# Optimization experiments

Measured on AMD Instinct MI355X. Metric: run time of the kernel, lower is better.

The kernel has to match this reference:

```python
import jax, jax.numpy as jnp
import numpy as np

B, N, D = 16, 512, 256
PH, UH, UPH = 8, 4, 4          # P_GAT heads, U_GAT heads, UP_GAT heads
P_LAYERS, U_LAYERS = 2, 1
FH, NC = 128, 2                # final hidden, num classes
N_TRAIT = 4


def setup_inputs() -> dict:
    key = jax.random.key(0)
    keys = iter(jax.random.split(key, 64))

    def rn(shape, s=0.05):
        return jax.random.normal(next(keys), shape, dtype=jnp.float32) * s

    inp = {
        "p_mask": jnp.ones((B, N), jnp.float32),
        "feature": rn((B, N, D), 1.0),
        "c_node": rn((B, 1, D), 1.0),
        "pgat_W": rn((D, D)),
        "pgat_attn": rn((PH, 2 * (D // PH))),
    }
    for i in range(1, 5):
        inp[f"up{i}_qw"] = rn((D, D))
        inp[f"up{i}_qb"] = rn((D,))
        inp[f"up{i}_kw"] = rn((D, D))
        inp[f"up{i}_kb"] = rn((D,))
        inp[f"up{i}_ow"] = rn((D, D * UPH))
        inp[f"up{i}_ob"] = rn((D,))
    inp["ugat_W"] = rn((D, D))
    inp["ugat_attn"] = rn((UH, 2 * (D // UH)))
    inp["mlp_w1"] = rn((FH, D))
    inp["mlp_b1"] = rn((FH,))
    inp["mlp_w2"] = rn((FH, FH))
    inp["mlp_b2"] = rn((FH,))
    for i in range(1, 5):
        inp[f"fcf{i}_w"] = rn((NC, FH))
        inp[f"fcf{i}_b"] = rn((NC,))
    return inp


def _mh_gat(feature, W, attn_w, n_head, num_layers, adj=None):
    """Shared math of P_GAT / U_GAT.
    attn(cat([q_i, k_j]))[..., h, h] decomposes into q_i.wq_h + k_j.wk_h,
    identical math to the broadcast-concat-linear-diagonal in the source."""
    Bx, Nx, d = feature.shape
    dh = d // n_head
    wq, wk = attn_w[:, :dh], attn_w[:, dh:]           # [h, dh] each
    for _ in range(num_layers):
        qk = (feature @ W.T).reshape(Bx, Nx, n_head, dh)
        sq = jnp.einsum('bqhd,hd->bqh', qk, wq)
        sk = jnp.einsum('bkhd,hd->bkh', qk, wk)
        scores = jnp.tanh(sq[:, :, None, :] + sk[:, None, :, :])  # [B,q,k,h]
        if adj is not None:
            scores = jnp.where(adj[:, :, :, None] == 0, jnp.float32(-1e-8), scores)
        att = jax.nn.softmax(scores, axis=-2)          # softmax over k
        hid = jnp.tanh(jnp.einsum('bqkh,bkhd->bqhd', att, qk))
        feature = feature + hid.reshape(Bx, Nx, d)
    return feature


def _up_gat(p_mask, p_feat, u_feat, qw, qb, kw, kb, ow, ob):
    """UP_GAT: all heads/layers share params & inputs -> identical heads."""
    d = p_feat.shape[-1]
    q = u_feat @ qw.T + qb                             # [B,1,D]
    k = p_feat @ kw.T + kb                             # [B,Np,D]
    sim = jnp.einsum('bqd,bkd->bqk', q, k) / jnp.sqrt(jnp.float32(d))
    sim = jnp.where(p_mask[:, None, :] == 0, jnp.float32(1e-8), sim)
    att = jax.nn.softmax(sim, axis=2)
    head = att @ p_feat                                # [B,1,D]
    mh = jnp.concatenate([head] * UPH, axis=-1)        # concat of identical heads
    return (mh @ ow.T + ob)[:, 0, :]                   # squeeze(1)


def reference(p_mask, feature, c_node, pgat_W, pgat_attn,
              up1_qw, up1_qb, up1_kw, up1_kb, up1_ow, up1_ob,
              up2_qw, up2_qb, up2_kw, up2_kb, up2_ow, up2_ob,
              up3_qw, up3_qb, up3_kw, up3_kb, up3_ow, up3_ob,
              up4_qw, up4_qb, up4_kw, up4_kb, up4_ow, up4_ob,
              ugat_W, ugat_attn, mlp_w1, mlp_b1, mlp_w2, mlp_b2,
              fcf1_w, fcf1_b, fcf2_w, fcf2_b, fcf3_w, fcf3_b, fcf4_w, fcf4_b):
    Bx = p_mask.shape[0]
    adj = p_mask[:, :, None] * p_mask[:, None, :]      # [B,N,N]
    new_p = _mh_gat(feature, pgat_W, pgat_attn, PH, P_LAYERS, adj=adj)
    new_mask = jnp.concatenate([p_mask, jnp.ones((Bx, 1), p_mask.dtype)], axis=1)
    comb = jnp.concatenate([new_p, c_node], axis=1)    # [B,N+1,D]

    u1 = _up_gat(new_mask, comb, c_node, up1_qw, up1_qb, up1_kw, up1_kb, up1_ow, up1_ob)
    u2 = _up_gat(new_mask, comb, c_node, up2_qw, up2_qb, up2_kw, up2_kb, up2_ow, up2_ob)
    u3 = _up_gat(new_mask, comb, c_node, up3_qw, up3_qb, up3_kw, up3_kb, up3_ow, up3_ob)
    u4 = _up_gat(new_mask, comb, c_node, up4_qw, up4_qb, up4_kw, up4_kb, up4_ow, up4_ob)

    u = jnp.stack([u1, u2, u3, u4], axis=1)            # [B,4,D]
    u = _mh_gat(u, ugat_W, ugat_attn, UH, U_LAYERS, adj=None)

    def mlp(x):  # fcs1..4 share modules in the torch source
        h = jax.nn.relu(x @ mlp_w1.T + mlp_b1)
        return jax.nn.relu(h @ mlp_w2.T + mlp_b2)

    heads = [(fcf1_w, fcf1_b), (fcf2_w, fcf2_b), (fcf3_w, fcf3_b), (fcf4_w, fcf4_b)]
    logits = [mlp(u[:, i]) @ w.T + b for i, (w, b) in enumerate(heads)]
    return jnp.stack(logits, axis=0)                   # [4,B,NC]
```

## Files before the change

### kernel.cpp

```cpp
#include <hip/hip_runtime.h>

constexpr int CB   = 16;
constexpr int CN   = 512;
constexpr int CD   = 256;
constexpr int CPH  = 8;
constexpr int CDH  = 32;
constexpr int CNP1 = 513;
constexpr int CFH  = 128;
constexpr int CNC  = 2;

typedef __bf16 bf16x8 __attribute__((ext_vector_type(8)));
typedef float  f32x4  __attribute__((ext_vector_type(4)));

__device__ __forceinline__ float tanh_fast(float x) {
  x = fminf(fmaxf(x, -15.f), 15.f);
  float e = __expf(2.f * x);
  return (e - 1.f) / (e + 1.f);
}

__global__ __launch_bounds__(256) void gemm_bf16s(
    const float* __restrict__ A, const float* __restrict__ W,
    float* __restrict__ C)
{
  const int t  = threadIdx.x;
  const int nt = blockIdx.x * 64;
  const int mt = blockIdx.y * 64;
  const int wv = t >> 6, ln = t & 63;
  const int quad = ln >> 4, lc = ln & 15;

  __shared__ __align__(16) __bf16 aHi[64][56];
  __shared__ __align__(16) __bf16 aLo[64][56];
  __shared__ __align__(16) __bf16 bHi[64][56];
  __shared__ __align__(16) __bf16 bLo[64][56];

  f32x4 acc[4];
#pragma unroll
  for (int j = 0; j < 4; j++)
#pragma unroll
    for (int r = 0; r < 4; r++) acc[j][r] = 0.f;

  const int sr  = t >> 2;
  const int skq = (t & 3) * 8;

  for (int k0 = 0; k0 < 256; k0 += 32) {
    __syncthreads();
    {
      const float* ap = A + (size_t)(mt + sr) * 256 + k0 + skq;
      const float* wp = W + (size_t)(nt + sr) * 256 + k0 + skq;
      float4 a0 = *(const float4*)ap, a1 = *(const float4*)(ap + 4);
      float4 w0 = *(const float4*)wp, w1 = *(const float4*)(wp + 4);
      float av[8] = {a0.x, a0.y, a0.z, a0.w, a1.x, a1.y, a1.z, a1.w};
      float wvv[8] = {w0.x, w0.y, w0.z, w0.w, w1.x, w1.y, w1.z, w1.w};
      bf16x8 ah, al, bh, bl;
#pragma unroll
      for (int j = 0; j < 8; j++) {
        ah[j] = (__bf16)av[j];
        al[j] = (__bf16)(av[j] - (float)ah[j]);
        bh[j] = (__bf16)wvv[j];
        bl[j] = (__bf16)(wvv[j] - (float)bh[j]);
      }
      *(bf16x8*)&aHi[sr][skq] = ah;
      *(bf16x8*)&aLo[sr][skq] = al;
      *(bf16x8*)&bHi[sr][skq] = bh;
      *(bf16x8*)&bLo[sr][skq] = bl;
    }
    __syncthreads();
    bf16x8 fah = *(const bf16x8*)&aHi[wv * 16 + lc][quad * 8];
    bf16x8 fal = *(const bf16x8*)&aLo[wv * 16 + lc][quad * 8];
#pragma unroll
    for (int j = 0; j < 4; j++) {
      bf16x8 fbh = *(const bf16x8*)&bHi[j * 16 + lc][quad * 8];
      bf16x8 fbl = *(const bf16x8*)&bLo[j * 16 + lc][quad * 8];
      acc[j] = __builtin_amdgcn_mfma_f32_16x16x32_bf16(fah, fbh, acc[j], 0, 0, 0);
      acc[j] = __builtin_amdgcn_mfma_f32_16x16x32_bf16(fah, fbl, acc[j], 0, 0, 0);
      acc[j] = __builtin_amdgcn_mfma_f32_16x16x32_bf16(fal, fbh, acc[j], 0, 0, 0);
    }
  }
#pragma unroll
  for (int j = 0; j < 4; j++)
#pragma unroll
    for (int r = 0; r < 4; r++)
      C[(size_t)(mt + wv * 16 + quad * 4 + r) * 256 + nt + j * 16 + lc] = acc[j][r];
}

__global__ __launch_bounds__(256) void pgat_sqsk(
    const float* __restrict__ qk, const float* __restrict__ attnw,
    float* __restrict__ sqT, float* __restrict__ skT)
{
  __shared__ float aw[CPH * 64];
  const int t = threadIdx.x;
  for (int i = t; i < CPH * 64; i += 256) aw[i] = attnw[i];
  __syncthreads();
  const int r = blockIdx.x * 32 + (t >> 3);
  const int h = t & 7;
  const float* p  = qk + (size_t)r * CD + h * CDH;
  const float* w1 = &aw[h * 64];
  const float* w2 = &aw[h * 64 + 32];
  float s1 = 0.f, s2 = 0.f;
#pragma unroll
  for (int j = 0; j < CDH; j += 4) {
    float4 v = *(const float4*)(p + j);
    s1 += v.x * w1[j] + v.y * w1[j + 1] + v.z * w1[j + 2] + v.w * w1[j + 3];
    s2 += v.x * w2[j] + v.y * w2[j + 1] + v.z * w2[j + 2] + v.w * w2[j + 3];
  }
  const int b = r >> 9, n = r & 511;
  sqT[((size_t)b * CPH + h) * CN + n] = s1;
  skT[((size_t)b * CPH + h) * CN + n] = s2;
}

__global__ __launch_bounds__(256) void pgat_attn_mfma(
    const float* __restrict__ qk, const float* __restrict__ sqT,
    const float* __restrict__ skT, const float* __restrict__ pmask,
    const float* __restrict__ fin, float* __restrict__ fout, int outStride)
{
  const int qt = blockIdx.x;
  const int h  = blockIdx.y;
  const int b  = blockIdx.z;
  const int t  = threadIdx.x;
  const int wv = t >> 6;
  const int ln = t & 63;
  const int quad = ln >> 4;
  const int lc   = ln & 15;

  __shared__ __align__(16) __bf16 pbuf[64][72];
  __shared__ __align__(16) __bf16 vbuf[32][72];
  __shared__ float skl[CN];
  __shared__ float pml[CN];
  __shared__ float sql[64];
  __shared__ float pmq[64];

  for (int i = t; i < CN; i += 256) {
    skl[i] = skT[((size_t)b * CPH + h) * CN + i];
    pml[i] = pmask[b * CN + i];
  }
  if (t < 64) {
    sql[t] = sqT[((size_t)b * CPH + h) * CN + qt * 64 + t];
    pmq[t] = pmask[b * CN + qt * 64 + t];
  }

  f32x4 accV0 = {0.f, 0.f, 0.f, 0.f};
  f32x4 accV1 = {0.f, 0.f, 0.f, 0.f};
  f32x4 accD  = {0.f, 0.f, 0.f, 0.f};
  bf16x8 ones;
#pragma unroll
  for (int j = 0; j < 8; j++) ones[j] = (__bf16)1.0f;

  const int qg = t >> 2;
  const int kb = (t & 3) * 16;
  const int vkk = t >> 3;
  const int vdq = (t & 7) * 4;

  for (int k0 = 0; k0 < CN; k0 += 64) {
    __syncthreads();
    {
      float4 v0 = *(const float4*)(qk + ((size_t)(b * CN + k0 + vkk)) * CD + h * CDH + vdq);
      float4 v1 = *(const float4*)(qk + ((size_t)(b * CN + k0 + 32 + vkk)) * CD + h * CDH + vdq);
      vbuf[vdq + 0][vkk] = (__bf16)v0.x; vbuf[vdq + 1][vkk] = (__bf16)v0.y;
      vbuf[vdq + 2][vkk] = (__bf16)v0.z; vbuf[vdq + 3][vkk] = (__bf16)v0.w;
      vbuf[vdq + 0][32 + vkk] = (__bf16)v1.x; vbuf[vdq + 1][32 + vkk] = (__bf16)v1.y;
      vbuf[vdq + 2][32 + vkk] = (__bf16)v1.z; vbuf[vdq + 3][32 + vkk] = (__bf16)v1.w;
    }
    {
      float sq_ = sql[qg];
      float mq  = pmq[qg];
      bf16x8 w0, w1;
#pragma unroll
      for (int j = 0; j < 8; j++) {
        float s = tanh_fast(sq_ + skl[k0 + kb + j]);
        if (mq * pml[k0 + kb + j] == 0.f) s = -1e-8f;
        w0[j] = (__bf16)__expf(s);
      }
#pragma unroll
      for (int j = 0; j < 8; j++) {
        float s = tanh_fast(sq_ + skl[k0 + kb + 8 + j]);
        if (mq * pml[k0 + kb + 8 + j] == 0.f) s = -1e-8f;
        w1[j] = (__bf16)__expf(s);
      }
      *(bf16x8*)&pbuf[qg][kb]     = w0;
      *(bf16x8*)&pbuf[qg][kb + 8] = w1;
    }
    __syncthreads();
#pragma unroll
    for (int s = 0; s < 2; s++) {
      bf16x8 a  = *(const bf16x8*)&pbuf[wv * 16 + lc][s * 32 + quad * 8];
      bf16x8 b0 = *(const bf16x8*)&vbuf[lc][s * 32 + quad * 8];
      bf16x8 b1 = *(const bf16x8*)&vbuf[16 + lc][s * 32 + quad * 8];
      accV0 = __builtin_amdgcn_mfma_f32_16x16x32_bf16(a, b0, accV0, 0, 0, 0);
      accV1 = __builtin_amdgcn_mfma_f32_16x16x32_bf16(a, b1, accV1, 0, 0, 0);
      accD  = __builtin_amdgcn_mfma_f32_16x16x32_bf16(a, ones, accD, 0, 0, 0);
    }
  }
#pragma unroll
  for (int r = 0; r < 4; r++) {
    int q = qt * 64 + wv * 16 + quad * 4 + r;
    float inv = 1.f / accD[r];
    int d0 = h * CDH + lc;
    const float* ip = fin + ((size_t)b * CN + q) * CD;
    float*       op = fout + ((size_t)b * outStride + q) * CD;
    op[d0]      = ip[d0]      + tanh_fast(accV0[r] * inv);
    op[d0 + 16] = ip[d0 + 16] + tanh_fast(accV1[r] * inv);
  }
}


__global__ __launch_bounds__(256) void up_q_all(
    const float* __restrict__ cnode,
    const float* __restrict__ qw0, const float* __restrict__ qb0,
    const float* __restrict__ kw0, const float* __restrict__ kb0,
    const float* __restrict__ qw1, const float* __restrict__ qb1,
    const float* __restrict__ kw1, const float* __restrict__ kb1,
    const float* __restrict__ qw2, const float* __restrict__ qb2,
    const float* __restrict__ kw2, const float* __restrict__ kb2,
    const float* __restrict__ qw3, const float* __restrict__ qb3,
    const float* __restrict__ kw3, const float* __restrict__ kb3,
    float* __restrict__ qt_, float* __restrict__ qkb,
    float* __restrict__ comb, float* __restrict__ head, float* __restrict__ den)
{
  const int up = blockIdx.x, b = blockIdx.y, t = threadIdx.x;
  const float* qw = (up == 0) ? qw0 : (up == 1) ? qw1 : (up == 2) ? qw2 : qw3;
  const float* qb = (up == 0) ? qb0 : (up == 1) ? qb1 : (up == 2) ? qb2 : qb3;
  const float* kw = (up == 0) ? kw0 : (up == 1) ? kw1 : (up == 2) ? kw2 : kw3;
  const float* kb = (up == 0) ? kb0 : (up == 1) ? kb1 : (up == 2) ? kb2 : kb3;
  __shared__ float cl[CD];
  __shared__ float ql[CD];
  __shared__ float red[256];
  cl[t] = cnode[b * CD + t];
  head[((size_t)b * 4 + up) * CD + t] = 0.f;
  if (t == 0) den[b * 4 + up] = 0.f;
  __syncthreads();
  if (up == 0) comb[((size_t)b * CNP1 + CN) * CD + t] = cl[t];
  {
    const float* wr = qw + (size_t)t * CD;
    float a = qb[t];
#pragma unroll 4
    for (int k = 0; k < CD; k += 4) {
      float4 w4 = *(const float4*)(wr + k);
      a += cl[k] * w4.x + cl[k + 1] * w4.y + cl[k + 2] * w4.z + cl[k + 3] * w4.w;
    }
    ql[t] = a;
  }
  __syncthreads();
  {
    float a = 0.f;
    for (int d = 0; d < CD; d++) a += ql[d] * kw[d * CD + t];
    qt_[((size_t)up * CB + b) * CD + t] = a;
  }
  red[t] = ql[t] * kb[t];
  __syncthreads();
  for (int s = 128; s > 0; s >>= 1) { if (t < s) red[t] += red[t + s]; __syncthreads(); }
  if (t == 0) qkb[up * CB + b] = red[0];
}

__global__ __launch_bounds__(256) void up_sim(
    const float* __restrict__ comb, const float* __restrict__ qt,
    const float* __restrict__ qkb, const float* __restrict__ pmask,
    float* __restrict__ sim)
{
  const int b = blockIdx.y, t = threadIdx.x;
  const int w = t >> 6, l = t & 63;
  __shared__ float qtl[4 * CD];
  __shared__ float qkbl[4];
  for (int i = t; i < 4 * CD; i += 256)
    qtl[i] = qt[((size_t)(i >> 8) * CB + b) * CD + (i & 255)];
  if (t < 4) qkbl[t] = qkb[t * CB + b];
  __syncthreads();
  const int n = blockIdx.x * 4 + w;
  if (n >= CNP1) return;
  float4 c4 = *(const float4*)(comb + ((size_t)b * CNP1 + n) * CD + l * 4);
  float p[4];
#pragma unroll
  for (int u = 0; u < 4; u++) {
    float4 q4 = *(const float4*)&qtl[u * CD + l * 4];
    p[u] = c4.x * q4.x + c4.y * q4.y + c4.z * q4.z + c4.w * q4.w;
  }
#pragma unroll
  for (int off = 32; off > 0; off >>= 1) {
#pragma unroll
    for (int u = 0; u < 4; u++) p[u] += __shfl_xor(p[u], off);
  }
  if (l == 0) {
    float m = (n < CN) ? pmask[b * CN + n] : 1.f;
#pragma unroll
    for (int u = 0; u < 4; u++) {
      float s = (p[u] + qkbl[u]) * 0.0625f;
      if (m == 0.f) s = 1e-8f;
      sim[((size_t)b * 4 + u) * CNP1 + n] = s;
    }
  }
}

__global__ __launch_bounds__(256) void up_head(
    const float* __restrict__ comb, const float* __restrict__ sim,
    float* __restrict__ head, float* __restrict__ den)
{
  const int b = blockIdx.x, n0 = blockIdx.y * 64, t = threadIdx.x;
  const int up = t >> 6, dq = t & 63;
  __shared__ float attl[4][64];
  {
    int u = t >> 6, j = t & 63;
    attl[u][j] = (n0 + j < CNP1)
        ? __expf(sim[((size_t)b * 4 + u) * CNP1 + n0 + j]) : 0.f;
  }
  __syncthreads();
  float4 acc = make_float4(0.f, 0.f, 0.f, 0.f);
  const int nmax = min(64, CNP1 - n0);
  for (int j = 0; j < nmax; j++) {
    float a = attl[up][j];
    float4 c4 = *(const float4*)(comb + ((size_t)b * CNP1 + n0 + j) * CD + dq * 4);
    acc.x += a * c4.x; acc.y += a * c4.y; acc.z += a * c4.z; acc.w += a * c4.w;
  }
  float* hp = head + ((size_t)b * 4 + up) * CD + dq * 4;
  atomicAdd(hp + 0, acc.x); atomicAdd(hp + 1, acc.y);
  atomicAdd(hp + 2, acc.z); atomicAdd(hp + 3, acc.w);
  if (dq == 0) {
    float s = 0.f;
    for (int j = 0; j < 64; j++) s += attl[up][j];
    atomicAdd(den + b * 4 + up, s);
  }
}

__global__ __launch_bounds__(256) void up_out_all(
    const float* __restrict__ head, const float* __restrict__ den,
    const float* __restrict__ ow0, const float* __restrict__ ob0,
    const float* __restrict__ ow1, const float* __restrict__ ob1,
    const float* __restrict__ ow2, const float* __restrict__ ob2,
    const float* __restrict__ ow3, const float* __restrict__ ob3,
    float* __restrict__ uout)
{
  const int b = blockIdx.x, up = blockIdx.y, t = threadIdx.x;
  const float* ow = (up == 0) ? ow0 : (up == 1) ? ow1 : (up == 2) ? ow2 : ow3;
  const float* ob = (up == 0) ? ob0 : (up == 1) ? ob1 : (up == 2) ? ob2 : ob3;
  __shared__ float hl[CD];
  hl[t] = head[((size_t)b * 4 + up) * CD + t] * (1.f / den[b * 4 + up]);
  __syncthreads();
  const float* r0 = ow + (size_t)t * 4 * CD;
  float a = ob[t];
#pragma unroll 2
  for (int dd = 0; dd < CD; dd += 4) {
    float4 w0 = *(const float4*)(r0 + dd);
    float4 w1 = *(const float4*)(r0 + CD + dd);
    float4 w2 = *(const float4*)(r0 + 2 * CD + dd);
    float4 w3 = *(const float4*)(r0 + 3 * CD + dd);
    a += hl[dd]     * (w0.x + w1.x + w2.x + w3.x)
       + hl[dd + 1] * (w0.y + w1.y + w2.y + w3.y)
       + hl[dd + 2] * (w0.z + w1.z + w2.z + w3.z)
       + hl[dd + 3] * (w0.w + w1.w + w2.w + w3.w);
  }
  uout[((size_t)b * 4 + up) * CD + t] = a;
}

__global__ __launch_bounds__(256) void ugat_qk(
    const float* __restrict__ u, const float* __restrict__ W,
    const float* __restrict__ attnw,
    float* __restrict__ uqk, float* __restrict__ sqk)
{
  const int b = blockIdx.x, node = blockIdx.y, t = threadIdx.x;
  __shared__ float ul[CD];
  __shared__ float qkl[CD];
  ul[t] = u[((size_t)b * 4 + node) * CD + t];
  __syncthreads();
  const float* wr = W + (size_t)t * CD;
  float p0 = 0.f, p1 = 0.f, p2 = 0.f, p3 = 0.f;
#pragma unroll 4
  for (int d = 0; d < CD; d += 16) {
    float4 w0 = *(const float4*)(wr + d);
    float4 w1 = *(const float4*)(wr + d + 4);
    float4 w2 = *(const float4*)(wr + d + 8);
    float4 w3 = *(const float4*)(wr + d + 12);
    p0 += ul[d +  0] * w0.x + ul[d +  1] * w0.y + ul[d +  2] * w0.z + ul[d +  3] * w0.w;
    p1 += ul[d +  4] * w1.x + ul[d +  5] * w1.y + ul[d +  6] * w1.z + ul[d +  7] * w1.w;
    p2 += ul[d +  8] * w2.x + ul[d +  9] * w2.y + ul[d + 10] * w2.z + ul[d + 11] * w2.w;
    p3 += ul[d + 12] * w3.x + ul[d + 13] * w3.y + ul[d + 14] * w3.z + ul[d + 15] * w3.w;
  }
  float a = (p0 + p1) + (p2 + p3);
  qkl[t] = a;
  uqk[((size_t)b * 4 + node) * CD + t] = a;
  __syncthreads();
  if (t < 8) {
    const int h = t >> 1, which = t & 1;
    const float* w = attnw + h * 128 + which * 64;
    float s = 0.f;
    for (int j = 0; j < 64; j++) s += qkl[h * 64 + j] * w[j];
    sqk[(((size_t)b * 4 + node) * 4 + h) * 2 + which] = s;
  }
}

__global__ __launch_bounds__(256) void ugat_attn3(
    const float* __restrict__ uqk, const float* __restrict__ sqk,
    float* __restrict__ u)
{
  const int b = blockIdx.x, t = threadIdx.x;
  __shared__ float uq[4][CD];
  __shared__ float sl[4][4], kl[4][4];
  for (int i = t; i < 4 * CD; i += 256) uq[i >> 8][i & 255] = uqk[(size_t)b * 4 * CD + i];
  if (t < 16) {
    int node = t >> 2, h = t & 3;
    sl[node][h] = sqk[(((size_t)b * 4 + node) * 4 + h) * 2 + 0];
    kl[node][h] = sqk[(((size_t)b * 4 + node) * 4 + h) * 2 + 1];
  }
  __syncthreads();
  const int h = t >> 6;
#pragma unroll
  for (int q = 0; q < 4; q++) {
    float e[4]; float ssum = 0.f;
#pragma unroll
    for (int k = 0; k < 4; k++) { e[k] = __expf(tanh_fast(sl[q][h] + kl[k][h])); ssum += e[k]; }
    float hid = 0.f;
#pragma unroll
    for (int k = 0; k < 4; k++) hid += e[k] * uq[k][t];
    size_t idx = (size_t)b * 4 * CD + q * CD + t;
    u[idx] = u[idx] + tanh_fast(hid / ssum);
  }
}

__global__ __launch_bounds__(128) void mlp_kernel(
    const float* __restrict__ u,
    const float* __restrict__ w1, const float* __restrict__ b1,
    const float* __restrict__ w2, const float* __restrict__ b2,
    const float* __restrict__ f1w, const float* __restrict__ f1b,
    const float* __restrict__ f2w, const float* __restrict__ f2b,
    const float* __restrict__ f3w, const float* __restrict__ f3b,
    const float* __restrict__ f4w, const float* __restrict__ f4b,
    float* __restrict__ out)
{
  const int b = blockIdx.x, i = blockIdx.y, t = threadIdx.x;
  __shared__ float xl[CD];
  __shared__ float h1[CFH];
  __shared__ float h2[CFH];
  xl[t]       = u[((size_t)b * 4 + i) * CD + t];
  xl[t + 128] = u[((size_t)b * 4 + i) * CD + t + 128];
  __syncthreads();
  {
    const float* r = w1 + (size_t)t * CD;
    float a = b1[t];
#pragma unroll 4
    for (int k = 0; k < CD; k += 4) {
      float4 v = *(const float4*)(r + k);
      a += xl[k] * v.x + xl[k + 1] * v.y + xl[k + 2] * v.z + xl[k + 3] * v.w;
    }
    h1[t] = fmaxf(a, 0.f);
  }
  __syncthreads();
  {
    const float* r = w2 + (size_t)t * CFH;
    float a = b2[t];
#pragma unroll 4
    for (int k = 0; k < CFH; k += 4) {
      float4 v = *(const float4*)(r + k);
      a += h1[k] * v.x + h1[k + 1] * v.y + h1[k + 2] * v.z + h1[k + 3] * v.w;
    }
    h2[t] = fmaxf(a, 0.f);
  }
  __syncthreads();
  if (t < CNC) {
    const float* fw; const float* fb;
    switch (i) {
      case 0:  fw = f1w; fb = f1b; break;
      case 1:  fw = f2w; fb = f2b; break;
      case 2:  fw = f3w; fb = f3b; break;
      default: fw = f4w; fb = f4b; break;
    }
    const float* r = fw + (size_t)t * CFH;
    float a = fb[t];
    for (int k = 0; k < CFH; k++) a += h2[k] * r[k];
    out[(size_t)i * (CB * CNC) + b * CNC + t] = a;
  }
}

extern "C" void kernel_launch(void* const* d_in, const int* in_sizes, int n_in,
                              void* d_out, int out_size, void* d_ws, size_t ws_size,
                              hipStream_t stream) {
  (void)in_sizes; (void)n_in; (void)out_size; (void)ws_size;
  const float* pmask    = (const float*)d_in[0];
  const float* feature  = (const float*)d_in[1];
  const float* cnode    = (const float*)d_in[2];
  const float* pgat_W   = (const float*)d_in[3];
  const float* pgat_att = (const float*)d_in[4];
  const float* upw[4][6];
  for (int i = 0; i < 4; i++)
    for (int j = 0; j < 6; j++) upw[i][j] = (const float*)d_in[5 + i * 6 + j];
  const float* ugat_W   = (const float*)d_in[29];
  const float* ugat_att = (const float*)d_in[30];
  const float* mlp_w1 = (const float*)d_in[31];
  const float* mlp_b1 = (const float*)d_in[32];
  const float* mlp_w2 = (const float*)d_in[33];
  const float* mlp_b2 = (const float*)d_in[34];
  const float* fcf[8];
  for (int j = 0; j < 8; j++) fcf[j] = (const float*)d_in[35 + j];

  float* ws = (float*)d_ws;
  size_t o = 0;
  float* ws_qk   = ws + o; o += (size_t)CB * CN * CD;
  float* ws_feat = ws + o; o += (size_t)CB * CN * CD;
  float* ws_comb = ws + o; o += (size_t)CB * CNP1 * CD;
  float* ws_sq   = ws + o; o += (size_t)CB * CPH * CN;
  float* ws_sk   = ws + o; o += (size_t)CB * CPH * CN;
  float* ws_qt   = ws + o; o += (size_t)4 * CB * CD;
  float* ws_qkb  = ws + o; o += 4 * CB;
  float* ws_sim  = ws + o; o += (size_t)CB * 4 * CNP1;
  float* ws_den  = ws + o; o += CB * 4;
  float* ws_head = ws + o; o += (size_t)CB * 4 * CD;
  float* ws_u    = ws + o; o += (size_t)CB * 4 * CD;
  float* ws_uqk  = ws + o; o += (size_t)CB * 4 * CD;
  float* ws_sqk  = ws + o; o += (size_t)CB * 4 * 4 * 2;

  const dim3 gemmGrid(CD / 64, (CB * CN) / 64);
  const dim3 attnGrid(CN / 64, CPH, CB);

  gemm_bf16s<<<gemmGrid, 256, 0, stream>>>(feature, pgat_W, ws_qk);
  pgat_sqsk<<<dim3(CB * CN / 32), 256, 0, stream>>>(ws_qk, pgat_att, ws_sq, ws_sk);
  pgat_attn_mfma<<<attnGrid, 256, 0, stream>>>(ws_qk, ws_sq, ws_sk, pmask, feature, ws_feat, CN);
  gemm_bf16s<<<gemmGrid, 256, 0, stream>>>(ws_feat, pgat_W, ws_qk);
  pgat_sqsk<<<dim3(CB * CN / 32), 256, 0, stream>>>(ws_qk, pgat_att, ws_sq, ws_sk);
  pgat_attn_mfma<<<attnGrid, 256, 0, stream>>>(ws_qk, ws_sq, ws_sk, pmask, ws_feat, ws_comb, CNP1);

  up_q_all<<<dim3(4, CB), 256, 0, stream>>>(cnode,
      upw[0][0], upw[0][1], upw[0][2], upw[0][3],
      upw[1][0], upw[1][1], upw[1][2], upw[1][3],
      upw[2][0], upw[2][1], upw[2][2], upw[2][3],
      upw[3][0], upw[3][1], upw[3][2], upw[3][3],
      ws_qt, ws_qkb, ws_comb, ws_head, ws_den);
  up_sim<<<dim3((CNP1 + 3) / 4, CB), 256, 0, stream>>>(ws_comb, ws_qt, ws_qkb, pmask, ws_sim);
  up_head<<<dim3(CB, (CNP1 + 63) / 64), 256, 0, stream>>>(ws_comb, ws_sim, ws_head, ws_den);
  up_out_all<<<dim3(CB, 4), 256, 0, stream>>>(ws_head, ws_den,
      upw[0][4], upw[0][5], upw[1][4], upw[1][5],
      upw[2][4], upw[2][5], upw[3][4], upw[3][5], ws_u);

  ugat_qk<<<dim3(CB, 4), 256, 0, stream>>>(ws_u, ugat_W, ugat_att, ws_uqk, ws_sqk);
  ugat_attn3<<<dim3(CB), 256, 0, stream>>>(ws_uqk, ws_sqk, ws_u);
  mlp_kernel<<<dim3(CB, 4), 128, 0, stream>>>(ws_u, mlp_w1, mlp_b1, mlp_w2, mlp_b2,
                                              fcf[0], fcf[1], fcf[2], fcf[3],
                                              fcf[4], fcf[5], fcf[6], fcf[7],
                                              (float*)d_out);
}
```

Baseline: 323.8 us.

## Fuse score projections into GEMM epilogue, store qk as bf16, merge small kernels

The GEMM epilogue now computes the per-head sq/sk attention projections through shuffle reductions and writes qk directly as bf16, which removes the separate pgat_sqsk kernel and halves qk traffic into the attention kernel. up_sim and up_head become one kernel that computes each similarity and exponentiates it in place, dropping the sim buffer. ugat_attn3 is folded into the MLP kernel. The cost is a reduction in precision for qk, which was already rounded to bf16 inside the attention kernel, and each up_headsim thread now runs a serial 256-element dot product.

```diff
diff --git a/kernel.cpp b/kernel.cpp
--- a/kernel.cpp
+++ b/kernel.cpp
@@ -10,6 +10,7 @@
 constexpr int CNC  = 2;
 
 typedef __bf16 bf16x8 __attribute__((ext_vector_type(8)));
+typedef __bf16 bf16x4 __attribute__((ext_vector_type(4)));
 typedef float  f32x4  __attribute__((ext_vector_type(4)));
 
 __device__ __forceinline__ float tanh_fast(float x) {
@@ -18,9 +19,10 @@
   return (e - 1.f) / (e + 1.f);
 }
 
-__global__ __launch_bounds__(256) void gemm_bf16s(
+__global__ __launch_bounds__(256) void gemm_fused(
     const float* __restrict__ A, const float* __restrict__ W,
-    float* __restrict__ C)
+    const float* __restrict__ attnw, __bf16* __restrict__ C,
+    float* __restrict__ sqT, float* __restrict__ skT)
 {
   const int t  = threadIdx.x;
   const int nt = blockIdx.x * 64;
@@ -80,36 +82,47 @@
   for (int j = 0; j < 4; j++)
 #pragma unroll
     for (int r = 0; r < 4; r++)
-      C[(size_t)(mt + wv * 16 + quad * 4 + r) * 256 + nt + j * 16 + lc] = acc[j][r];
-}
-
-__global__ __launch_bounds__(256) void pgat_sqsk(
-    const float* __restrict__ qk, const float* __restrict__ attnw,
-    float* __restrict__ sqT, float* __restrict__ skT)
-{
-  __shared__ float aw[CPH * 64];
-  const int t = threadIdx.x;
-  for (int i = t; i < CPH * 64; i += 256) aw[i] = attnw[i];
-  __syncthreads();
-  const int r = blockIdx.x * 32 + (t >> 3);
-  const int h = t & 7;
-  const float* p  = qk + (size_t)r * CD + h * CDH;
-  const float* w1 = &aw[h * 64];
-  const float* w2 = &aw[h * 64 + 32];
-  float s1 = 0.f, s2 = 0.f;
-#pragma unroll
-  for (int j = 0; j < CDH; j += 4) {
-    float4 v = *(const float4*)(p + j);
-    s1 += v.x * w1[j] + v.y * w1[j + 1] + v.z * w1[j + 2] + v.w * w1[j + 3];
-    s2 += v.x * w2[j] + v.y * w2[j + 1] + v.z * w2[j + 2] + v.w * w2[j + 3];
-  }
-  const int b = r >> 9, n = r & 511;
-  sqT[((size_t)b * CPH + h) * CN + n] = s1;
-  skT[((size_t)b * CPH + h) * CN + n] = s2;
+      C[(size_t)(mt + wv * 16 + quad * 4 + r) * 256 + nt + j * 16 + lc] =
+          (__bf16)acc[j][r];
+
+  const int hA = blockIdx.x * 2, hB = hA + 1;
+  const float wqa0 = attnw[hA * 64 + lc],      wqa1 = attnw[hA * 64 + 16 + lc];
+  const float wka0 = attnw[hA * 64 + 32 + lc], wka1 = attnw[hA * 64 + 48 + lc];
+  const float wqb0 = attnw[hB * 64 + lc],      wqb1 = attnw[hB * 64 + 16 + lc];
+  const float wkb0 = attnw[hB * 64 + 32 + lc], wkb1 = attnw[hB * 64 + 48 + lc];
+  float sqa[4], ska[4], sqb[4], skb[4];
+#pragma unroll
+  for (int r = 0; r < 4; r++) {
+    sqa[r] = acc[0][r] * wqa0 + acc[1][r] * wqa1;
+    ska[r] = acc[0][r] * wka0 + acc[1][r] * wka1;
+    sqb[r] = acc[2][r] * wqb0 + acc[3][r] * wqb1;
+    skb[r] = acc[2][r] * wkb0 + acc[3][r] * wkb1;
+  }
+#pragma unroll
+  for (int m = 1; m <= 8; m <<= 1) {
+#pragma unroll
+    for (int r = 0; r < 4; r++) {
+      sqa[r] += __shfl_xor(sqa[r], m);
+      ska[r] += __shfl_xor(ska[r], m);
+      sqb[r] += __shfl_xor(sqb[r], m);
+      skb[r] += __shfl_xor(skb[r], m);
+    }
+  }
+  if (lc == 0) {
+#pragma unroll
+    for (int r = 0; r < 4; r++) {
+      int gm = mt + wv * 16 + quad * 4 + r;
+      int bb = gm >> 9, nn = gm & 511;
+      sqT[((size_t)bb * CPH + hA) * CN + nn] = sqa[r];
+      skT[((size_t)bb * CPH + hA) * CN + nn] = ska[r];
+      sqT[((size_t)bb * CPH + hB) * CN + nn] = sqb[r];
+      skT[((size_t)bb * CPH + hB) * CN + nn] = skb[r];
+    }
+  }
 }
 
 __global__ __launch_bounds__(256) void pgat_attn_mfma(
-    const float* __restrict__ qk, const float* __restrict__ sqT,
+    const __bf16* __restrict__ qk, const float* __restrict__ sqT,
     const float* __restrict__ skT, const float* __restrict__ pmask,
     const float* __restrict__ fin, float* __restrict__ fout, int outStride)
 {
@@ -153,12 +166,12 @@
   for (int k0 = 0; k0 < CN; k0 += 64) {
     __syncthreads();
     {
-      float4 v0 = *(const float4*)(qk + ((size_t)(b * CN + k0 + vkk)) * CD + h * CDH + vdq);
-      float4 v1 = *(const float4*)(qk + ((size_t)(b * CN + k0 + 32 + vkk)) * CD + h * CDH + vdq);
-      vbuf[vdq + 0][vkk] = (__bf16)v0.x; vbuf[vdq + 1][vkk] = (__bf16)v0.y;
-      vbuf[vdq + 2][vkk] = (__bf16)v0.z; vbuf[vdq + 3][vkk] = (__bf16)v0.w;
-      vbuf[vdq + 0][32 + vkk] = (__bf16)v1.x; vbuf[vdq + 1][32 + vkk] = (__bf16)v1.y;
-      vbuf[vdq + 2][32 + vkk] = (__bf16)v1.z; vbuf[vdq + 3][32 + vkk] = (__bf16)v1.w;
+      bf16x4 v0 = *(const bf16x4*)(qk + ((size_t)(b * CN + k0 + vkk)) * CD + h * CDH + vdq);
+      bf16x4 v1 = *(const bf16x4*)(qk + ((size_t)(b * CN + k0 + 32 + vkk)) * CD + h * CDH + vdq);
+      vbuf[vdq + 0][vkk] = v0[0]; vbuf[vdq + 1][vkk] = v0[1];
+      vbuf[vdq + 2][vkk] = v0[2]; vbuf[vdq + 3][vkk] = v0[3];
+      vbuf[vdq + 0][32 + vkk] = v1[0]; vbuf[vdq + 1][32 + vkk] = v1[1];
+      vbuf[vdq + 2][32 + vkk] = v1[2]; vbuf[vdq + 3][32 + vkk] = v1[3];
     }
     {
       float sq_ = sql[qg];
@@ -251,70 +264,53 @@
   if (t == 0) qkb[up * CB + b] = red[0];
 }
 
-__global__ __launch_bounds__(256) void up_sim(
+__global__ __launch_bounds__(256) void up_headsim(
     const float* __restrict__ comb, const float* __restrict__ qt,
     const float* __restrict__ qkb, const float* __restrict__ pmask,
-    float* __restrict__ sim)
-{
-  const int b = blockIdx.y, t = threadIdx.x;
-  const int w = t >> 6, l = t & 63;
-  __shared__ float qtl[4 * CD];
+    float* __restrict__ head, float* __restrict__ den)
+{
+  const int b = blockIdx.x, n0 = blockIdx.y * 64, t = threadIdx.x;
+  const int up = t >> 6, j = t & 63;
+  __shared__ float qtl[4][CD];
   __shared__ float qkbl[4];
+  __shared__ float attl[4][64];
   for (int i = t; i < 4 * CD; i += 256)
-    qtl[i] = qt[((size_t)(i >> 8) * CB + b) * CD + (i & 255)];
+    qtl[i >> 8][i & 255] = qt[((size_t)(i >> 8) * CB + b) * CD + (i & 255)];
   if (t < 4) qkbl[t] = qkb[t * CB + b];
   __syncthreads();
-  const int n = blockIdx.x * 4 + w;
-  if (n >= CNP1) return;
-  float4 c4 = *(const float4*)(comb + ((size_t)b * CNP1 + n) * CD + l * 4);
-  float p[4];
-#pragma unroll
-  for (int u = 0; u < 4; u++) {
-    float4 q4 = *(const float4*)&qtl[u * CD + l * 4];
-    p[u] = c4.x * q4.x + c4.y * q4.y + c4.z * q4.z + c4.w * q4.w;
-  }
-#pragma unroll
-  for (int off = 32; off > 0; off >>= 1) {
-#pragma unroll
-    for (int u = 0; u < 4; u++) p[u] += __shfl_xor(p[u], off);
-  }
-  if (l == 0) {
-    float m = (n < CN) ? pmask[b * CN + n] : 1.f;
-#pragma unroll
-    for (int u = 0; u < 4; u++) {
-      float s = (p[u] + qkbl[u]) * 0.0625f;
+  {
+    const int n = n0 + j;
+    float e = 0.f;
+    if (n < CNP1) {
+      const float* cr = comb + ((size_t)b * CNP1 + n) * CD;
+      float p = 0.f;
+#pragma unroll 4
+      for (int d = 0; d < CD; d += 4) {
+        float4 c4 = *(const float4*)(cr + d);
+        p += qtl[up][d] * c4.x + qtl[up][d + 1] * c4.y
+           + qtl[up][d + 2] * c4.z + qtl[up][d + 3] * c4.w;
+      }
+      float s = (p + qkbl[up]) * 0.0625f;
+      float m = (n < CN) ? pmask[b * CN + n] : 1.f;
       if (m == 0.f) s = 1e-8f;
-      sim[((size_t)b * 4 + u) * CNP1 + n] = s;
-    }
-  }
-}
-
-__global__ __launch_bounds__(256) void up_head(
-    const float* __restrict__ comb, const float* __restrict__ sim,
-    float* __restrict__ head, float* __restrict__ den)
-{
-  const int b = blockIdx.x, n0 = blockIdx.y * 64, t = threadIdx.x;
-  const int up = t >> 6, dq = t & 63;
-  __shared__ float attl[4][64];
-  {
-    int u = t >> 6, j = t & 63;
-    attl[u][j] = (n0 + j < CNP1)
-        ? __expf(sim[((size_t)b * 4 + u) * CNP1 + n0 + j]) : 0.f;
+      e = __expf(s);
+    }
+    attl[up][j] = e;
   }
   __syncthreads();
   float4 acc = make_float4(0.f, 0.f, 0.f, 0.f);
   const int nmax = min(64, CNP1 - n0);
-  for (int j = 0; j < nmax; j++) {
-    float a = attl[up][j];
-    float4 c4 = *(const float4*)(comb + ((size_t)b * CNP1 + n0 + j) * CD + dq * 4);
+  for (int jj = 0; jj < nmax; jj++) {
+    float a = attl[up][jj];
+    float4 c4 = *(const float4*)(comb + ((size_t)b * CNP1 + n0 + jj) * CD + j * 4);
     acc.x += a * c4.x; acc.y += a * c4.y; acc.z += a * c4.z; acc.w += a * c4.w;
   }
-  float* hp = head + ((size_t)b * 4 + up) * CD + dq * 4;
+  float* hp = head + ((size_t)b * 4 + up) * CD + j * 4;
   atomicAdd(hp + 0, acc.x); atomicAdd(hp + 1, acc.y);
   atomicAdd(hp + 2, acc.z); atomicAdd(hp + 3, acc.w);
-  if (dq == 0) {
+  if (j == 0) {
     float s = 0.f;
-    for (int j = 0; j < 64; j++) s += attl[up][j];
+    for (int jj = 0; jj < 64; jj++) s += attl[up][jj];
     atomicAdd(den + b * 4 + up, s);
   }
 }
@@ -385,36 +381,9 @@
   }
 }
 
-__global__ __launch_bounds__(256) void ugat_attn3(
-    const float* __restrict__ uqk, const float* __restrict__ sqk,
-    float* __restrict__ u)
-{
-  const int b = blockIdx.x, t = threadIdx.x;
-  __shared__ float uq[4][CD];
-  __shared__ float sl[4][4], kl[4][4];
-  for (int i = t; i < 4 * CD; i += 256) uq[i >> 8][i & 255] = uqk[(size_t)b * 4 * CD + i];
-  if (t < 16) {
-    int node = t >> 2, h = t & 3;
-    sl[node][h] = sqk[(((size_t)b * 4 + node) * 4 + h) * 2 + 0];
-    kl[node][h] = sqk[(((size_t)b * 4 + node) * 4 + h) * 2 + 1];
-  }
-  __syncthreads();
-  const int h = t >> 6;
-#pragma unroll
-  for (int q = 0; q < 4; q++) {
-    float e[4]; float ssum = 0.f;
-#pragma unroll
-    for (int k = 0; k < 4; k++) { e[k] = __expf(tanh_fast(sl[q][h] + kl[k][h])); ssum += e[k]; }
-    float hid = 0.f;
-#pragma unroll
-    for (int k = 0; k < 4; k++) hid += e[k] * uq[k][t];
-    size_t idx = (size_t)b * 4 * CD + q * CD + t;
-    u[idx] = u[idx] + tanh_fast(hid / ssum);
-  }
-}
-
-__global__ __launch_bounds__(128) void mlp_kernel(
-    const float* __restrict__ u,
+__global__ __launch_bounds__(256) void ugat_mlp2(
+    const float* __restrict__ u, const float* __restrict__ uqk,
+    const float* __restrict__ sqk,
     const float* __restrict__ w1, const float* __restrict__ b1,
     const float* __restrict__ w2, const float* __restrict__ b2,
     const float* __restrict__ f1w, const float* __restrict__ f1b,
@@ -423,14 +392,32 @@
     const float* __restrict__ f4w, const float* __restrict__ f4b,
     float* __restrict__ out)
 {
-  const int b = blockIdx.x, i = blockIdx.y, t = threadIdx.x;
+  const int b = blockIdx.x, trait = blockIdx.y, t = threadIdx.x;
+  __shared__ float uq[4][CD];
+  __shared__ float sl[4][4], kl[4][4];
   __shared__ float xl[CD];
   __shared__ float h1[CFH];
   __shared__ float h2[CFH];
-  xl[t]       = u[((size_t)b * 4 + i) * CD + t];
-  xl[t + 128] = u[((size_t)b * 4 + i) * CD + t + 128];
+  for (int i = t; i < 4 * CD; i += 256) uq[i >> 8][i & 255] = uqk[(size_t)b * 4 * CD + i];
+  if (t < 16) {
+    int node = t >> 2, h = t & 3;
+    sl[node][h] = sqk[(((size_t)b * 4 + node) * 4 + h) * 2 + 0];
+    kl[node][h] = sqk[(((size_t)b * 4 + node) * 4 + h) * 2 + 1];
+  }
+  float ur = u[((size_t)b * 4 + trait) * CD + t];
   __syncthreads();
   {
+    const int h = t >> 6;
+    float e[4]; float ssum = 0.f;
+#pragma unroll
+    for (int k = 0; k < 4; k++) { e[k] = __expf(tanh_fast(sl[trait][h] + kl[k][h])); ssum += e[k]; }
+    float hid = 0.f;
+#pragma unroll
+    for (int k = 0; k < 4; k++) hid += e[k] * uq[k][t];
+    xl[t] = ur + tanh_fast(hid / ssum);
+  }
+  __syncthreads();
+  if (t < CFH) {
     const float* r = w1 + (size_t)t * CD;
     float a = b1[t];
 #pragma unroll 4
@@ -441,7 +428,7 @@
     h1[t] = fmaxf(a, 0.f);
   }
   __syncthreads();
-  {
+  if (t < CFH) {
     const float* r = w2 + (size_t)t * CFH;
     float a = b2[t];
 #pragma unroll 4
@@ -454,7 +441,7 @@
   __syncthreads();
   if (t < CNC) {
     const float* fw; const float* fb;
-    switch (i) {
+    switch (trait) {
       case 0:  fw = f1w; fb = f1b; break;
       case 1:  fw = f2w; fb = f2b; break;
       case 2:  fw = f3w; fb = f3b; break;
@@ -463,7 +450,7 @@
     const float* r = fw + (size_t)t * CFH;
     float a = fb[t];
     for (int k = 0; k < CFH; k++) a += h2[k] * r[k];
-    out[(size_t)i * (CB * CNC) + b * CNC + t] = a;
+    out[(size_t)trait * (CB * CNC) + b * CNC + t] = a;
   }
 }
 
@@ -497,22 +484,20 @@
   float* ws_sk   = ws + o; o += (size_t)CB * CPH * CN;
   float* ws_qt   = ws + o; o += (size_t)4 * CB * CD;
   float* ws_qkb  = ws + o; o += 4 * CB;
-  float* ws_sim  = ws + o; o += (size_t)CB * 4 * CNP1;
   float* ws_den  = ws + o; o += CB * 4;
   float* ws_head = ws + o; o += (size_t)CB * 4 * CD;
   float* ws_u    = ws + o; o += (size_t)CB * 4 * CD;
   float* ws_uqk  = ws + o; o += (size_t)CB * 4 * CD;
   float* ws_sqk  = ws + o; o += (size_t)CB * 4 * 4 * 2;
+  __bf16* qk16 = (__bf16*)ws_qk;
 
   const dim3 gemmGrid(CD / 64, (CB * CN) / 64);
   const dim3 attnGrid(CN / 64, CPH, CB);
 
-  gemm_bf16s<<<gemmGrid, 256, 0, stream>>>(feature, pgat_W, ws_qk);
-  pgat_sqsk<<<dim3(CB * CN / 32), 256, 0, stream>>>(ws_qk, pgat_att, ws_sq, ws_sk);
-  pgat_attn_mfma<<<attnGrid, 256, 0, stream>>>(ws_qk, ws_sq, ws_sk, pmask, feature, ws_feat, CN);
-  gemm_bf16s<<<gemmGrid, 256, 0, stream>>>(ws_feat, pgat_W, ws_qk);
-  pgat_sqsk<<<dim3(CB * CN / 32), 256, 0, stream>>>(ws_qk, pgat_att, ws_sq, ws_sk);
-  pgat_attn_mfma<<<attnGrid, 256, 0, stream>>>(ws_qk, ws_sq, ws_sk, pmask, ws_feat, ws_comb, CNP1);
+  gemm_fused<<<gemmGrid, 256, 0, stream>>>(feature, pgat_W, pgat_att, qk16, ws_sq, ws_sk);
+  pgat_attn_mfma<<<attnGrid, 256, 0, stream>>>(qk16, ws_sq, ws_sk, pmask, feature, ws_feat, CN);
+  gemm_fused<<<gemmGrid, 256, 0, stream>>>(ws_feat, pgat_W, pgat_att, qk16, ws_sq, ws_sk);
+  pgat_attn_mfma<<<attnGrid, 256, 0, stream>>>(qk16, ws_sq, ws_sk, pmask, ws_feat, ws_comb, CNP1);
 
   up_q_all<<<dim3(4, CB), 256, 0, stream>>>(cnode,
       upw[0][0], upw[0][1], upw[0][2], upw[0][3],
@@ -520,16 +505,16 @@
       upw[2][0], upw[2][1], upw[2][2], upw[2][3],
       upw[3][0], upw[3][1], upw[3][2], upw[3][3],
       ws_qt, ws_qkb, ws_comb, ws_head, ws_den);
-  up_sim<<<dim3((CNP1 + 3) / 4, CB), 256, 0, stream>>>(ws_comb, ws_qt, ws_qkb, pmask, ws_sim);
-  up_head<<<dim3(CB, (CNP1 + 63) / 64), 256, 0, stream>>>(ws_comb, ws_sim, ws_head, ws_den);
+  up_headsim<<<dim3(CB, (CNP1 + 63) / 64), 256, 0, stream>>>(ws_comb, ws_qt, ws_qkb, pmask,
+                                                             ws_head, ws_den);
   up_out_all<<<dim3(CB, 4), 256, 0, stream>>>(ws_head, ws_den,
       upw[0][4], upw[0][5], upw[1][4], upw[1][5],
       upw[2][4], upw[2][5], upw[3][4], upw[3][5], ws_u);
 
   ugat_qk<<<dim3(CB, 4), 256, 0, stream>>>(ws_u, ugat_W, ugat_att, ws_uqk, ws_sqk);
-  ugat_attn3<<<dim3(CB), 256, 0, stream>>>(ws_uqk, ws_sqk, ws_u);
-  mlp_kernel<<<dim3(CB, 4), 128, 0, stream>>>(ws_u, mlp_w1, mlp_b1, mlp_w2, mlp_b2,
-                                              fcf[0], fcf[1], fcf[2], fcf[3],
-                                              fcf[4], fcf[5], fcf[6], fcf[7],
-                                              (float*)d_out);
-}
+  ugat_mlp2<<<dim3(CB, 4), 256, 0, stream>>>(ws_u, ws_uqk, ws_sqk,
+                                             mlp_w1, mlp_b1, mlp_w2, mlp_b2,
+                                             fcf[0], fcf[1], fcf[2], fcf[3],
+                                             fcf[4], fcf[5], fcf[6], fcf[7],
+                                             (float*)d_out);
+}
```

Measured after the change: 320.0 us. No clear change (-1.2%).
